# Performance work log

Hardware: AMD Instinct MI355X
Metric: run time of the kernel (lower is better)

The kernel has to match this reference:

```python
import jax, jax.numpy as jnp
from jax import lax
import numpy as np

B, C, H, W = 4, 256, 64, 64
O, KH, KW = 256, 3, 3
STR, PAD, DIL = 1, 1, 1
K = KH * KW
EPS = 1e-5


def setup_inputs() -> dict:
    key = jax.random.key(0)
    ks = jax.random.split(key, 8)
    fan = 1.0 / np.sqrt(C * KH * KW)
    return {
        "input_x": jax.random.normal(ks[0], (B, C, H, W), jnp.float32),
        # offset-generating conv (DeformConv2dPack style): 2*K channels of (dy, dx)
        "w_offset": jax.random.normal(ks[1], (2 * K, C, KH, KW), jnp.float32) * 0.01,
        "b_offset": jnp.zeros((2 * K,), jnp.float32),
        # deformable conv weight / bias
        "weight": jax.random.normal(ks[2], (O, C, KH, KW), jnp.float32) * fan,
        "bias": jax.random.normal(ks[3], (O,), jnp.float32) * 0.01,
        # BatchNorm2d params + running stats (inference mode)
        "gamma": jax.random.normal(ks[4], (O,), jnp.float32) * 0.1 + 1.0,
        "beta": jax.random.normal(ks[5], (O,), jnp.float32) * 0.1,
        "run_mean": jax.random.normal(ks[6], (O,), jnp.float32) * 0.1,
        "run_var": jax.random.uniform(ks[7], (O,), jnp.float32, 0.5, 1.5),
    }


def _bilinear_sample(img, y, x):
    """img: [B,C,H,W]; y,x: [B,K,Ho,Wo] float sample coords. Zero outside."""
    y0 = jnp.floor(y)
    x0 = jnp.floor(x)
    ly = y - y0
    lx = x - x0
    y0i = y0.astype(jnp.int32)
    x0i = x0.astype(jnp.int32)
    y1i = y0i + 1
    x1i = x0i + 1

    def valid(yi, xi):
        return ((yi >= 0) & (yi < H) & (xi >= 0) & (xi < W)).astype(img.dtype)

    # per-corner interpolation weights, zeroed when the corner is out of bounds
    w00 = (1 - ly) * (1 - lx) * valid(y0i, x0i)
    w01 = (1 - ly) * lx * valid(y0i, x1i)
    w10 = ly * (1 - lx) * valid(y1i, x0i)
    w11 = ly * lx * valid(y1i, x1i)

    y0c = jnp.clip(y0i, 0, H - 1)
    y1c = jnp.clip(y1i, 0, H - 1)
    x0c = jnp.clip(x0i, 0, W - 1)
    x1c = jnp.clip(x1i, 0, W - 1)

    gather = jax.vmap(lambda im, yi, xi: im[:, yi, xi])  # -> [B,C,K,Ho,Wo]
    out = gather(img, y0c, x0c) * w00[:, None]
    out = out + gather(img, y0c, x1c) * w01[:, None]
    out = out + gather(img, y1c, x0c) * w10[:, None]
    out = out + gather(img, y1c, x1c) * w11[:, None]
    return out  # [B,C,K,Ho,Wo]


def reference(input_x, w_offset, b_offset, weight, bias, gamma, beta, run_mean, run_var):
    # 1) generate offsets with a regular conv (DeformConv2dPack conv_offset)
    offset = lax.conv_general_dilated(
        input_x, w_offset, (STR, STR), [(PAD, PAD), (PAD, PAD)],
        rhs_dilation=(DIL, DIL), dimension_numbers=("NCHW", "OIHW", "NCHW"))
    offset = offset + b_offset[None, :, None, None]  # [B, 2K, Ho, Wo]
    Ho, Wo = offset.shape[2], offset.shape[3]
    off = offset.reshape(B, K, 2, Ho, Wo)
    dy, dx = off[:, :, 0], off[:, :, 1]  # [B,K,Ho,Wo]

    # 2) base sampling grid for each kernel tap
    ky, kx = jnp.meshgrid(jnp.arange(KH), jnp.arange(KW), indexing="ij")
    base_y = (jnp.arange(Ho) * STR - PAD)[None, :, None] + (ky.reshape(-1) * DIL)[:, None, None]
    base_x = (jnp.arange(Wo) * STR - PAD)[None, None, :] + (kx.reshape(-1) * DIL)[:, None, None]
    y = base_y.astype(input_x.dtype) + dy  # [B,K,Ho,Wo]
    x = base_x.astype(input_x.dtype) + dx

    # 3) bilinear-sampled im2col then dense contraction
    sampled = _bilinear_sample(input_x, y, x)  # [B,C,K,Ho,Wo]
    out = jnp.einsum("bckhw,ock->bohw", sampled, weight.reshape(O, C, K))
    out = out + bias[None, :, None, None]

    # 4) BatchNorm (inference, running stats) + ReLU
    inv = gamma / jnp.sqrt(run_var + EPS)
    out = out * inv[None, :, None, None] + (beta - run_mean * inv)[None, :, None, None]
    return jax.nn.relu(out)
```

## Files before the change

kernel.cpp:

```cpp
#include <hip/hip_runtime.h>
#include <math.h>

typedef __attribute__((ext_vector_type(8))) short b8;
typedef __attribute__((ext_vector_type(4))) float f4;
typedef float f4u __attribute__((ext_vector_type(4), aligned(4)));
typedef _Float16 h8 __attribute__((ext_vector_type(8)));
typedef _Float16 h2 __attribute__((ext_vector_type(2)));

#define XT2   0
#define OF2   2097152
#define WH2   2392064
#define WL2   2428928
#define AF2   3571712
#define BF2   3866624

#define BARRIER_RELAX() do {                                   \
    asm volatile("s_waitcnt lgkmcnt(0)" ::: "memory");         \
    __builtin_amdgcn_s_barrier();                              \
  } while (0)

__device__ inline ushort f2bf(float f) {
  uint u = __float_as_uint(f);
  return (ushort)((u + 0x7FFFu + ((u >> 16) & 1u)) >> 16);
}
__device__ inline h2 u2h2(uint u) { union { uint u; h2 h; } x; x.u = u; return x.h; }
__device__ inline uint h22u(h2 h) { union { uint u; h2 h; } x; x.h = h; return x.u; }
__device__ inline uint duph(float f) {
  union { _Float16 h; ushort u; } x; x.h = (_Float16)f;
  return ((uint)x.u << 16) | x.u;
}

__global__ __launch_bounds__(256) void prep0_k(
    const float* __restrict__ wof, const float* __restrict__ bias,
    const float* __restrict__ gamma, const float* __restrict__ beta,
    const float* __restrict__ mean, const float* __restrict__ var,
    float* __restrict__ ws) {
  const int tid = blockIdx.x * 256 + threadIdx.x;
  ((f4*)(ws + OF2))[tid] = f4{0.f, 0.f, 0.f, 0.f};
  if (tid < 256) {
    const float iv = gamma[tid] * rsqrtf(var[tid] + 1e-5f);
    ws[BF2 + tid] = bias[tid] * iv + beta[tid] - mean[tid] * iv;
  }
  if (tid < 9216) {
    const int l2  = tid & 63;
    const int mt  = (tid >> 6) & 1;
    const int i2  = tid >> 7;
    const int cg2 = i2 / 9;
    const int kk2 = i2 - cg2 * 9;
    const int oc  = (mt << 4) + (l2 & 15);
    const int cb2 = (cg2 << 5) + ((l2 >> 4) << 3);
    b8 ph, pl;
#pragma unroll
    for (int j = 0; j < 8; ++j) {
      const float v = (oc < 18) ? wof[((oc << 8) + cb2 + j) * 9 + kk2] : 0.f;
      const ushort h = f2bf(v);
      const float hf = __uint_as_float((uint)h << 16);
      ph[j] = (short)h;
      pl[j] = (short)f2bf(v - hf);
    }
    *(b8*)((short*)(ws + WH2) + tid * 8) = ph;
    *(b8*)((short*)(ws + WL2) + tid * 8) = pl;
  }
}

__global__ __launch_bounds__(256, 4) void mid_k(
    const float* __restrict__ x, const float* __restrict__ w,
    const float* __restrict__ gamma, const float* __restrict__ var,
    float* __restrict__ ws) {
  __shared__ __align__(16) ushort Xh[3][66][40];
  __shared__ __align__(16) ushort Xl[3][66][40];
  const int bid = blockIdx.x;
  const int t   = threadIdx.x;

  if (bid >= 3072) {
    const int tid = (bid - 3072) * 256 + t;
    const int l  = tid & 63;
    const int ot = (tid >> 6) & 15;
    const int f  = tid >> 10;
    const int o  = (ot << 4) + (l & 15);
    const float inv = gamma[o] * rsqrtf(var[o] + 1e-5f);
    const int s  = f & 1;
    const int g  = f >> 1;
    const int cw = g / 9;
    const int kk = g - cw * 9;
    const int cb = (cw << 6) + (s << 5) + ((l >> 4) << 3);
    h8 pk;
#pragma unroll
    for (int j = 0; j < 8; ++j)
      pk[j] = (_Float16)(w[((o << 8) + cb + j) * 9 + kk] * inv);
    *(h8*)((_Float16*)(ws + AF2) + tid * 8) = pk;
    return;
  }

  const int r = bid % 3;
  const int g = bid / 3;
  if (r != 2) {
    const int id  = ((g << 1) + r) * 256 + t;
    const int p   = id & 4095;
    const int cg8 = (id >> 12) & 31;
    const int b   = id >> 17;
    const float* xp = x + (((long)(b * 256 + cg8 * 8)) << 12) + p;
    _Float16* xt = (_Float16*)(ws + XT2);
    h8 pk;
#pragma unroll
    for (int j = 0; j < 8; ++j) pk[j] = (_Float16)xp[(long)j << 12];
    *(h8*)(xt + ((((long)(b << 12) + p)) << 8) + (cg8 << 3)) = pk;
    return;
  }

  const int q   = g >> 8;
  const int b   = (g >> 6) & 3;
  const int ho  = g & 63;
  const int l   = t & 63;
  const int wv  = t >> 6;
  const short* afh = (const short*)(ws + WH2);
  const short* afl = (const short*)(ws + WL2);

  for (int u = t; u < 240; u += 256) {
    const int row = u / 80, rem = u % 80;
    const int col = (rem >= 40) ? 65 : 0;
    const int c   = rem % 40;
    Xh[row][col][c] = 0;
    Xl[row][col][c] = 0;
  }

  f4 acc[2];
  acc[0] = f4{0.f, 0.f, 0.f, 0.f};
  acc[1] = f4{0.f, 0.f, 0.f, 0.f};

  const int cidx = t >> 3;
  const int j8   = t & 7;
  const float* xc = x + ((long)b << 20) + ((long)cidx << 12);
  const int col = (wv << 4) + (l & 15);
  const int qc  = (l >> 4) << 3;

  for (int it = 0; it < 2; ++it) {
    const int cg = (q << 1) + it;
    __syncthreads();
    const float* xg = xc + ((long)(cg << 5) << 12);
#pragma unroll
    for (int rep = 0; rep < 6; ++rep) {
      const int fi   = (rep << 3) + j8;
      const int row  = fi >> 4;
      const int colf = (fi & 15) << 2;
      const int y = ho - 1 + row;
      f4u v = {0.f, 0.f, 0.f, 0.f};
      if (y >= 0 && y <= 63) v = *(const f4u*)(xg + (y << 6) + colf);
#pragma unroll
      for (int qq = 0; qq < 4; ++qq) {
        const ushort h = f2bf(v[qq]);
        const float hf = __uint_as_float((uint)h << 16);
        Xh[row][colf + 1 + qq][cidx] = h;
        Xl[row][colf + 1 + qq][cidx] = f2bf(v[qq] - hf);
      }
    }
    __syncthreads();
#pragma unroll
    for (int kk = 0; kk < 9; ++kk) {
      const int ky = kk / 3, kx = kk - ky * 3;
      const int i  = cg * 9 + kk;
      const b8 ah0 = *(const b8*)(afh + ((((i << 1) + 0) << 6) + l) * 8);
      const b8 ah1 = *(const b8*)(afh + ((((i << 1) + 1) << 6) + l) * 8);
      const b8 al0 = *(const b8*)(afl + ((((i << 1) + 0) << 6) + l) * 8);
      const b8 al1 = *(const b8*)(afl + ((((i << 1) + 1) << 6) + l) * 8);
      const b8 bh = *(const b8*)&Xh[ky][col + kx][qc];
      const b8 bl = *(const b8*)&Xl[ky][col + kx][qc];
      acc[0] = __builtin_amdgcn_mfma_f32_16x16x32_bf16(ah0, bh, acc[0], 0, 0, 0);
      acc[0] = __builtin_amdgcn_mfma_f32_16x16x32_bf16(ah0, bl, acc[0], 0, 0, 0);
      acc[0] = __builtin_amdgcn_mfma_f32_16x16x32_bf16(al0, bh, acc[0], 0, 0, 0);
      acc[1] = __builtin_amdgcn_mfma_f32_16x16x32_bf16(ah1, bh, acc[1], 0, 0, 0);
      acc[1] = __builtin_amdgcn_mfma_f32_16x16x32_bf16(ah1, bl, acc[1], 0, 0, 0);
      acc[1] = __builtin_amdgcn_mfma_f32_16x16x32_bf16(al1, bh, acc[1], 0, 0, 0);
    }
  }

  const int wo = col;
  const int q4 = (l >> 4) << 2;
#pragma unroll
  for (int mt = 0; mt < 2; ++mt)
#pragma unroll
    for (int rr = 0; rr < 4; ++rr) {
      const int oc = (mt << 4) + q4 + rr;
      if (oc < 18)
        atomicAdd(&ws[OF2 + ((b * 18 + oc) << 12) + (ho << 6) + wo],
                  acc[mt][rr]);
    }
}

__global__ __launch_bounds__(512, 2) void deform_gemm_f16b(
    const float* __restrict__ ws, const float* __restrict__ bof,
    float* __restrict__ out) {
  __shared__ __align__(16) uint Bs[3][64][32];
  __shared__ uint4 dW[576];
  __shared__ int4  dP[576];

  const int t     = threadIdx.x;
  const int bid   = blockIdx.x;
  const int xcd   = bid & 7;
  const int batch = xcd >> 1;
  const int half  = xcd & 1;
  const int j     = bid >> 3;
  const int sp0   = (half << 11) + (j << 6);
  const int l     = t & 63;
  const int wv    = t >> 6;

  const int sn  = ((wv & 3) << 4) | (l & 15);
  const int cg8 = ((wv >> 2) << 2) | (l >> 4);
  const uint* xtu = (const uint*)(ws + XT2) + ((long)batch << 19);
  const _Float16* af = (const _Float16*)(ws + AF2);

  for (int u = t; u < 576; u += 512) {
    const int kk = u >> 6, s = u & 63;
    const int sp = sp0 + s;
    const int ho = sp >> 6, wo = sp & 63;
    const int ky = kk / 3, kx = kk - ky * 3;
    const float dy =
        ws[OF2 + ((batch * 18 + (kk << 1)) << 12) + sp] + bof[kk << 1];
    const float dx =
        ws[OF2 + ((batch * 18 + (kk << 1) + 1) << 12) + sp] + bof[(kk << 1) + 1];
    const float py = (float)(ho - 1 + ky) + dy;
    const float px = (float)(wo - 1 + kx) + dx;
    const float y0f = floorf(py), x0f = floorf(px);
    const float ly = py - y0f, lx = px - x0f;
    const int y0 = (int)y0f, x0 = (int)x0f;
    const int y1 = y0 + 1, x1 = x0 + 1;
    const float vy0 = (y0 >= 0 && y0 < 64) ? 1.f : 0.f;
    const float vy1 = (y1 >= 0 && y1 < 64) ? 1.f : 0.f;
    const float vx0 = (x0 >= 0 && x0 < 64) ? 1.f : 0.f;
    const float vx1 = (x1 >= 0 && x1 < 64) ? 1.f : 0.f;
    const int y0c = min(max(y0, 0), 63), y1c = min(max(y1, 0), 63);
    const int x0c = min(max(x0, 0), 63), x1c = min(max(x1, 0), 63);
    uint4 wv4;
    wv4.x = duph((1.f - ly) * (1.f - lx) * vy0 * vx0);
    wv4.y = duph((1.f - ly) * lx * vy0 * vx1);
    wv4.z = duph(ly * (1.f - lx) * vy1 * vx0);
    wv4.w = duph(ly * lx * vy1 * vx1);
    int4 pv;
    pv.x = (y0c << 6) + x0c;
    pv.y = (y0c << 6) + x1c;
    pv.z = (y1c << 6) + x0c;
    pv.w = (y1c << 6) + x1c;
    dW[u] = wv4;
    dP[u] = pv;
  }
  __syncthreads();

  f4 acc[2][4];
#pragma unroll
  for (int m = 0; m < 2; ++m)
#pragma unroll
    for (int nt = 0; nt < 4; ++nt) acc[m][nt] = f4{0.f, 0.f, 0.f, 0.f};

  uint4 cset0[4], cset1[4];
  uint4 w0v, w1v, wq; int4 pq;
  h8 aA[2][2], aN[2][2];
  int kkd, kkg, cwg, bufc;

#define FRDD(W_, P_, KK_) do { const int u_ = ((KK_) << 6) + sn;             \
    W_ = dW[u_]; P_ = dP[u_]; } while (0)

#define FGATH(DST_, P_) do {                                                 \
    const int co_ = (cwg << 5) + (cg8 << 2);                                 \
    DST_[0] = *(const uint4*)(xtu + ((P_).x << 7) + co_);                    \
    DST_[1] = *(const uint4*)(xtu + ((P_).y << 7) + co_);                    \
    DST_[2] = *(const uint4*)(xtu + ((P_).z << 7) + co_);                    \
    DST_[3] = *(const uint4*)(xtu + ((P_).w << 7) + co_);                    \
  } while (0)

#define FCOMB(CS_, WV_, BUF_) do {                                           \
    const h2 wc0_ = u2h2((WV_).x), wc1_ = u2h2((WV_).y);                     \
    const h2 wc2_ = u2h2((WV_).z), wc3_ = u2h2((WV_).w);                     \
    uint4 r_;                                                                \
    r_.x = h22u(u2h2(CS_[0].x) * wc0_ + u2h2(CS_[1].x) * wc1_ +              \
                u2h2(CS_[2].x) * wc2_ + u2h2(CS_[3].x) * wc3_);              \
    r_.y = h22u(u2h2(CS_[0].y) * wc0_ + u2h2(CS_[1].y) * wc1_ +              \
                u2h2(CS_[2].y) * wc2_ + u2h2(CS_[3].y) * wc3_);              \
    r_.z = h22u(u2h2(CS_[0].z) * wc0_ + u2h2(CS_[1].z) * wc1_ +              \
                u2h2(CS_[2].z) * wc2_ + u2h2(CS_[3].z) * wc3_);              \
    r_.w = h22u(u2h2(CS_[0].w) * wc0_ + u2h2(CS_[1].w) * wc1_ +              \
                u2h2(CS_[2].w) * wc2_ + u2h2(CS_[3].w) * wc3_);              \
    *(uint4*)&Bs[BUF_][sn][(cg8 ^ (sn & 7)) << 2] = r_;                      \
  } while (0)

#define FLOADA(I_, DST_) do {                                                \
    _Pragma("unroll")                                                        \
    for (int m = 0; m < 2; ++m)                                              \
      _Pragma("unroll")                                                      \
      for (int s = 0; s < 2; ++s) {                                          \
        const int f_ = ((I_) << 1) + s;                                      \
        DST_[m][s] = *(const h8*)(af +                                       \
            ((((f_ << 4) + (wv << 1) + m) << 6) + l) * 8);                   \
      }                                                                      \
  } while (0)

#define FMFMA(AC_, BUF_) do {                                                \
    h8 bB_[4][2];                                                            \
    _Pragma("unroll")                                                        \
    for (int nt = 0; nt < 4; ++nt)                                           \
      _Pragma("unroll")                                                      \
      for (int s = 0; s < 2; ++s) {                                          \
        const int snr_ = (nt << 4) + (l & 15);                               \
        const int ph_  = (((s << 2) + (l >> 4)) ^ (snr_ & 7)) << 2;          \
        bB_[nt][s] = *(const h8*)&Bs[BUF_][snr_][ph_];                       \
      }                                                                      \
    _Pragma("unroll")                                                        \
    for (int m = 0; m < 2; ++m)                                              \
      _Pragma("unroll")                                                      \
      for (int nt = 0; nt < 4; ++nt) {                                       \
        acc[m][nt] = __builtin_amdgcn_mfma_f32_16x16x32_f16(                 \
            AC_[m][0], bB_[nt][0], acc[m][nt], 0, 0, 0);                     \
        acc[m][nt] = __builtin_amdgcn_mfma_f32_16x16x32_f16(                 \
            AC_[m][1], bB_[nt][1], acc[m][nt], 0, 0, 0);                     \
      }                                                                      \
  } while (0)

#define FBODY(I_, AC_, AN_, CC_, WC_, CN_, WN_) do {                         \
    if ((I_) < 34) {                                                         \
      WN_ = wq; FGATH(CN_, pq);                                              \
      kkg++; if (kkg == 9) { kkg = 0; cwg++; }                               \
    }                                                                        \
    if ((I_) < 33) { FRDD(wq, pq, kkd); kkd = (kkd == 8) ? 0 : kkd + 1; }    \
    const int bufn_ = (bufc == 2) ? 0 : bufc + 1;                            \
    FMFMA(AC_, bufc);                                                        \
    if ((I_) < 35) {                                                         \
      FLOADA((I_) + 1, AN_);                                                 \
      FCOMB(CC_, WC_, bufn_);                                                \
    }                                                                        \
    bufc = bufn_;                                                            \
    BARRIER_RELAX();                                                         \
  } while (0)

  {
    uint4 wA; int4 pA;
    cwg = 0;
    FRDD(wA, pA, 0);
    FGATH(cset0, pA);
    FRDD(w1v, pA, 1);
    FGATH(cset1, pA);
    FRDD(wq, pq, 2);
    FLOADA(0, aA);
    FCOMB(cset0, wA, 0);
    kkd = 3; kkg = 2; bufc = 0;
  }
  BARRIER_RELAX();

  for (int i = 0; i < 36; i += 2) {
    FBODY(i,     aA, aN, cset1, w1v, cset0, w0v);
    FBODY(i + 1, aN, aA, cset0, w0v, cset1, w1v);
  }

  const float* bfold = ws + BF2;
  const int quad = l >> 4;
#pragma unroll
  for (int m = 0; m < 2; ++m) {
    const int ob = (((wv << 1) + m) << 4) + (quad << 2);
    const f4 bf = *(const f4*)&bfold[ob];
#pragma unroll
    for (int nt = 0; nt < 4; ++nt) {
      const int sp = sp0 + (nt << 4) + (l & 15);
#pragma unroll
      for (int rr = 0; rr < 4; ++rr) {
        out[(((batch << 8) + ob + rr) << 12) + sp] =
            fmaxf(acc[m][nt][rr] + bf[rr], 0.f);
      }
    }
  }
}

extern "C" void kernel_launch(void* const* d_in, const int* in_sizes, int n_in,
                              void* d_out, int out_size, void* d_ws, size_t ws_size,
                              hipStream_t stream) {
  const float* x     = (const float*)d_in[0];
  const float* wof   = (const float*)d_in[1];
  const float* bof   = (const float*)d_in[2];
  const float* w     = (const float*)d_in[3];
  const float* bias  = (const float*)d_in[4];
  const float* gamma = (const float*)d_in[5];
  const float* beta  = (const float*)d_in[6];
  const float* mean  = (const float*)d_in[7];
  const float* var   = (const float*)d_in[8];
  float* out = (float*)d_out;
  float* ws  = (float*)d_ws;

  hipLaunchKernelGGL(prep0_k, dim3(288), dim3(256), 0, stream,
                     wof, bias, gamma, beta, mean, var, ws);
  hipLaunchKernelGGL(mid_k, dim3(3360), dim3(256), 0, stream,
                     x, w, gamma, var, ws);
  hipLaunchKernelGGL(deform_gemm_f16b, dim3(256), dim3(512), 0, stream,
                     ws, bof, out);
}
```

Before: 150.4 us.

## Deepen LDS B-buffer ring to four stages and halve block barriers

```diff
diff --git a/kernel.cpp b/kernel.cpp
--- a/kernel.cpp
+++ b/kernel.cpp
@@ -190,7 +190,7 @@
 __global__ __launch_bounds__(512, 2) void deform_gemm_f16b(
     const float* __restrict__ ws, const float* __restrict__ bof,
     float* __restrict__ out) {
-  __shared__ __align__(16) uint Bs[3][64][32];
+  __shared__ __align__(16) uint Bs[4][64][32];
   __shared__ uint4 dW[576];
   __shared__ int4  dP[576];
 
@@ -254,7 +254,7 @@
   uint4 cset0[4], cset1[4];
   uint4 w0v, w1v, wq; int4 pq;
   h8 aA[2][2], aN[2][2];
-  int kkd, kkg, cwg, bufc;
+  int kkd, kkg, cwg;
 
 #define FRDD(W_, P_, KK_) do { const int u_ = ((KK_) << 6) + sn;             \
     W_ = dW[u_]; P_ = dP[u_]; } while (0)
@@ -314,40 +314,43 @@
       }                                                                      \
   } while (0)
 
-#define FBODY(I_, AC_, AN_, CC_, WC_, CN_, WN_) do {                         \
-    if ((I_) < 34) {                                                         \
-      WN_ = wq; FGATH(CN_, pq);                                              \
-      kkg++; if (kkg == 9) { kkg = 0; cwg++; }                               \
-    }                                                                        \
-    if ((I_) < 33) { FRDD(wq, pq, kkd); kkd = (kkd == 8) ? 0 : kkd + 1; }    \
-    const int bufn_ = (bufc == 2) ? 0 : bufc + 1;                            \
-    FMFMA(AC_, bufc);                                                        \
-    if ((I_) < 35) {                                                         \
-      FLOADA((I_) + 1, AN_);                                                 \
-      FCOMB(CC_, WC_, bufn_);                                                \
-    }                                                                        \
-    bufc = bufn_;                                                            \
+#define FBODY2(J_) do {                                                      \
+    const int je_ = (J_);                                                    \
+    if (je_ < 33) { w0v = wq; FGATH(cset0, pq);                              \
+      kkg++; if (kkg == 9) { kkg = 0; cwg++; } }                             \
+    if (je_ < 32) { FRDD(wq, pq, kkd); kkd = (kkd == 8) ? 0 : kkd + 1; }     \
+    __builtin_amdgcn_s_setprio(1);                                           \
+    FMFMA(aA, (je_ & 3));                                                    \
+    __builtin_amdgcn_s_setprio(0);                                           \
+    if (je_ < 35) FLOADA(je_ + 1, aN);                                       \
+    if (je_ < 34) FCOMB(cset1, w1v, ((je_ + 2) & 3));                        \
+    const int jo_ = (J_) + 1;                                                \
+    if (jo_ < 33) { w1v = wq; FGATH(cset1, pq);                              \
+      kkg++; if (kkg == 9) { kkg = 0; cwg++; } }                             \
+    if (jo_ < 32) { FRDD(wq, pq, kkd); kkd = (kkd == 8) ? 0 : kkd + 1; }     \
+    __builtin_amdgcn_s_setprio(1);                                           \
+    FMFMA(aN, (jo_ & 3));                                                    \
+    __builtin_amdgcn_s_setprio(0);                                           \
+    if (jo_ < 35) FLOADA(jo_ + 1, aA);                                       \
+    if (jo_ < 34) FCOMB(cset0, w0v, ((jo_ + 2) & 3));                        \
     BARRIER_RELAX();                                                         \
   } while (0)
 
   {
-    uint4 wA; int4 pA;
+    uint4 wA, wB; int4 pA;
     cwg = 0;
-    FRDD(wA, pA, 0);
-    FGATH(cset0, pA);
-    FRDD(w1v, pA, 1);
-    FGATH(cset1, pA);
-    FRDD(wq, pq, 2);
+    FRDD(wA, pA, 0); FGATH(cset0, pA);
+    FRDD(wB, pA, 1); FGATH(cset1, pA);
+    FCOMB(cset0, wA, 0);
+    FCOMB(cset1, wB, 1);
+    FRDD(w1v, pA, 2); FGATH(cset1, pA);
+    FRDD(wq, pq, 3);
     FLOADA(0, aA);
-    FCOMB(cset0, wA, 0);
-    kkd = 3; kkg = 2; bufc = 0;
+    kkd = 4; kkg = 3;
   }
   BARRIER_RELAX();
 
-  for (int i = 0; i < 36; i += 2) {
-    FBODY(i,     aA, aN, cset1, w1v, cset0, w0v);
-    FBODY(i + 1, aN, aA, cset0, w0v, cset1, w1v);
-  }
+  for (int i = 0; i < 36; i += 2) FBODY2(i);
 
   const float* bfold = ws + BF2;
   const int quad = l >> 4;
```

New measurement: 149.5 us. No clear change (-0.7%).
